# Optimization experiments

Measured on AMD Instinct MI355X. Metric: run time of the kernel, lower is better.

Reference implementation:

```python
import jax, jax.numpy as jnp
import numpy as np

K = 9            # connections per output pixel
GA = 2           # global additional samples
RA = 2           # relative additional samples
VS = 4 + GA + RA # 2^rank neighbours + sampled
REGION = 12      # int(0.25 * 48) per spatial dim
MMULT = 0.1
MIN_SIGMA = 0.05
SIGMA_SCALE = 0.05
SIGMA_BOOST = 2.0


def setup_inputs() -> dict:
    key = jax.random.key(0)
    ks = jax.random.split(key, 8)
    b, cin, h, w = 8, 128, 48, 48
    cout = 256
    hidden = cin * 4

    def lin_init(k, fan_out, fan_in):
        bound = 1.0 / np.sqrt(fan_in)
        kw, kb = jax.random.split(k)
        W = jax.random.uniform(kw, (fan_out, fan_in), minval=-bound, maxval=bound, dtype=jnp.float32)
        bb = jax.random.uniform(kb, (fan_out,), minval=-bound, maxval=bound, dtype=jnp.float32)
        return W, bb

    x = jax.random.normal(ks[0], (b, cin, h, w), dtype=jnp.float32)
    W1, b1 = lin_init(ks[1], hidden, 2)          # toparams layer 1 (adaptive=False -> 2 coord inputs)
    W2, b2 = lin_init(ks[2], 3 * K, hidden)      # toparams layer 2 -> k means (2d) + k sigmas
    Wu, bu = lin_init(ks[3], cout, K * cin)      # unify linear
    gints = jax.random.randint(ks[4], (b, h, w, K, GA, 2), 0, h, dtype=jnp.int32)      # global samples (h==w)
    roff = jax.random.randint(ks[5], (b, h, w, K, RA, 2), 0, REGION, dtype=jnp.int32)  # relative offsets
    return {"x": x, "W1": W1, "b1": b1, "W2": W2, "b2": b2, "Wu": Wu, "bu": bu,
            "gints": gints, "roff": roff}


def reference(x, W1, b1, W2, b2, Wu, bu, gints, roff):
    b, c, h, w = x.shape
    s = jnp.array([h, w], dtype=x.dtype)                       # spatial range per dim
    s_int = jnp.array([h, w], dtype=jnp.int32)

    # normalized coordinate grid in [0,1], (h, w, 2) with [.,.,0]=row, [.,.,1]=col
    rows = jnp.arange(h, dtype=x.dtype) / (h - 1)
    cols = jnp.arange(w, dtype=x.dtype) / (w - 1)
    coords = jnp.stack(jnp.meshgrid(rows, cols, indexing='ij'), axis=-1)

    # hypernetwork: per-pixel coords -> K 2d mean offsets + K sigmas
    inp = jnp.broadcast_to(coords, (b, h, w, 2))
    hid = jax.nn.relu(inp @ W1.T + b1)
    params = hid @ W2.T + b2                                   # (b,h,w,3K)
    means_raw = params[..., :2 * K].reshape(b, h, w, K, 2)
    sig_raw = params[..., 2 * K:]                              # (b,h,w,K)

    # mids: inverse of the sigmoid scaling applied to the pixel's own coordinate
    pix = coords * (s - 1)                                     # pixel coordinates
    sc = pix / (s - 1) * 0.9999 + 0.00005
    mids = jnp.log(sc / (1.0 - sc))                            # (h,w,2)

    # transform_means: sigmoid -> [0, s-1]
    means = jax.nn.sigmoid(mids[None, :, :, None, :] + MMULT * means_raw) * (s - 1)  # (b,h,w,K,2)
    # transform_sigmas: softplus(. + boost) + min, per-dim scale, then sigma_scale
    sigmas = (jax.nn.softplus(sig_raw + SIGMA_BOOST) + MIN_SIGMA)[..., None] * s * SIGMA_SCALE  # (b,h,w,K,2)

    # ---- integer index generation (non-differentiable) ----
    fl = jnp.floor(jax.lax.stop_gradient(means)).astype(jnp.int32)   # (b,h,w,K,2)
    combos = jnp.array([[0, 0], [0, 1], [1, 0], [1, 1]], dtype=jnp.int32)
    neigh = fl[..., None, :] + combos                                 # (b,h,w,K,4,2)
    rel = fl[..., None, :] + roff - REGION // 2                       # (b,h,w,K,RA,2)
    ints = jnp.concatenate([neigh, gints, rel], axis=-2) % s_int      # (b,h,w,K,VS,2)

    # duplicate masking: zero any tuple that occurred earlier along VS
    eq = jnp.all(ints[..., :, None, :] == ints[..., None, :, :], axis=-1)  # (...,VS,VS)
    lower = jnp.tril(jnp.ones((VS, VS), dtype=bool), k=-1)
    dups = jnp.any(eq & lower, axis=-1)                               # (b,h,w,K,VS)

    # unnormalized gaussian densities of integer points under (means, sigmas)
    diff = (ints.astype(x.dtype) - means[..., None, :]) / sigmas[..., None, :]
    props = jnp.exp(-0.5 * jnp.sum(diff * diff, axis=-1))             # (b,h,w,K,VS)
    props = jnp.where(dups, jnp.zeros((), x.dtype), props)
    weights = props / jnp.sum(props, axis=-1, keepdims=True)          # mvalues are all-ones

    # irregular gather of input channel vectors at sampled pixels
    lin = ints[..., 0] * w + ints[..., 1]                             # (b,h,w,K,VS)
    flat = x.transpose(0, 2, 3, 1).reshape(b, h * w, c)
    feats = flat[jnp.arange(b)[:, None], lin.reshape(b, -1)]          # (b, h*w*K*VS, c)
    feats = feats.reshape(b, h, w, K, VS, c)

    feats = jnp.einsum('bhwkvc,bhwkv->bhwkc', feats, weights)         # weighted reduce over VS
    feats = feats.reshape(b, h, w, K * c)
    out = feats @ Wu.T + bu                                           # unify linear
    return out.transpose(0, 3, 1, 2)                                  # (b, cout, h, w)
```

## Files before the change

### kernel.cpp

```cpp
#include <hip/hip_runtime.h>
#include <hip/hip_bf16.h>
#include <hip/hip_fp16.h>

#define BB 8
#define CIN 128
#define HH 48
#define WW 48
#define HW 2304
#define KK 9
#define COUT 256
#define KC 1152
#define MM 18432
#define MT 16
#define SFP 136

#define LIGHT_BARRIER() asm volatile("s_waitcnt lgkmcnt(0)\n\ts_barrier" ::: "memory")

typedef short bf16x8_t __attribute__((ext_vector_type(8)));
typedef float f32x4_t  __attribute__((ext_vector_type(4)));

static __device__ __forceinline__ float b2f(short u) {
    union { unsigned int i; float f; } c;
    c.i = ((unsigned int)(unsigned short)u) << 16;
    return c.f;
}

__global__ __launch_bounds__(256) void prep_kernel(
    const float* __restrict__ x, __hip_bfloat16* __restrict__ xT,
    const float* __restrict__ Wu, bf16x8_t* __restrict__ Bp,
    const float* __restrict__ W1, const float* __restrict__ b1,
    const float* __restrict__ W2, const float* __restrict__ b2,
    float* __restrict__ means, float* __restrict__ sigmas, int* __restrict__ fls)
{
    int bid = blockIdx.x;
    int t = threadIdx.x;

    if (bid < 576) {
        __shared__ float tile[64][65];
        int ij0 = (bid % 36) * 64;
        int c0  = ((bid / 36) % 2) * 64;
        int b   = bid / 72;
        int ijl = t & 63, cl = t >> 6;
        #pragma unroll
        for (int i = 0; i < 16; i++) {
            int cc = i*4 + cl;
            tile[cc][ijl] = x[(size_t)(b*CIN + c0 + cc) * HW + ij0 + ijl];
        }
        __syncthreads();
        int cl2 = t & 63, ijl2 = t >> 6;
        #pragma unroll
        for (int i = 0; i < 16; i++) {
            int ij = i*4 + ijl2;
            xT[(size_t)(b*HW + ij0 + ij) * CIN + c0 + cl2] = __float2bfloat16(tile[cl2][ij]);
        }
    } else if (bid < 720) {
        int idx = (bid - 576) * 256 + t;
        int lane = idx & 63;
        int rest = idx >> 6;
        int ksub = rest % 36, tile16 = rest / 36;
        const float* src = Wu + (size_t)(tile16*16 + (lane & 15)) * KC
                              + ksub*32 + (lane >> 4)*8;
        union { bf16x8_t v; __hip_bfloat16 h[8]; } o;
        #pragma unroll
        for (int j = 0; j < 8; j++) o.h[j] = __float2bfloat16(src[j]);
        Bp[idx] = o.v;
    } else {
        int wave = t >> 6, lane = t & 63;
        int p = (bid - 720) * 4 + wave;
        int iy = p / WW, ix = p % WW;
        float ryf = (float)iy / 47.0f;
        float rxf = (float)ix / 47.0f;
        double ry = (double)ryf, rx = (double)rxf;

        double h[8];
        #pragma unroll
        for (int jj = 0; jj < 8; jj++) {
            int j = lane*8 + jj;
            double v = ry * (double)W1[j*2+0] + rx * (double)W1[j*2+1] + (double)b1[j];
            h[jj] = v > 0.0 ? v : 0.0;
        }
        double par[27];
        #pragma unroll
        for (int o = 0; o < 27; o++) {
            const float4* w4 = (const float4*)(W2 + (size_t)o*512 + lane*8);
            float4 wa = w4[0], wb = w4[1];
            double s = (double)wa.x*h[0] + (double)wa.y*h[1]
                     + (double)wa.z*h[2] + (double)wa.w*h[3]
                     + (double)wb.x*h[4] + (double)wb.y*h[5]
                     + (double)wb.z*h[6] + (double)wb.w*h[7];
            par[o] = s;
        }
        #pragma unroll
        for (int o = 0; o < 27; o++) {
            #pragma unroll
            for (int d = 1; d < 64; d <<= 1)
                par[o] += __shfl_xor(par[o], d, 64);
            par[o] += (double)b2[o];
        }
        if (lane < KK) {
            int k = lane;
            double scy = ry * 0.9999 + 5e-05;
            double scx = rx * 0.9999 + 5e-05;
            double midy = log(scy / (1.0 - scy));
            double midx = log(scx / (1.0 - scx));
            double zy = midy + 0.1 * par[2*k+0];
            double zx = midx + 0.1 * par[2*k+1];
            double my = 47.0 / (1.0 + exp(-zy));
            double mx = 47.0 / (1.0 + exp(-zx));
            double sr = par[18 + k] + 2.0;
            double sp = (sr > 0.0 ? sr : 0.0) + log1p(exp(-fabs(sr)));
            double sg = (sp + 0.05) * 48.0 * 0.05;
            means[(p*KK + k)*2 + 0] = (float)my;
            means[(p*KK + k)*2 + 1] = (float)mx;
            sigmas[p*KK + k] = (float)sg;
            fls[(p*KK + k)*2 + 0] = (int)floor(my);
            fls[(p*KK + k)*2 + 1] = (int)floor(mx);
        }
    }
}

__global__ __launch_bounds__(256, 4) void fused_kernel(
    const float* __restrict__ means, const float* __restrict__ sigmas,
    const int* __restrict__ fls, const int* __restrict__ gints,
    const int* __restrict__ roff, const short* __restrict__ xT,
    const bf16x8_t* __restrict__ Bp, const float* __restrict__ bu,
    float* __restrict__ out)
{
    __shared__ unsigned int s_tap[KK*MT*8];
    __shared__ __align__(16) short s_feat[2][MT*SFP];

    int t = threadIdx.x;
    int b   = blockIdx.x & 7;
    int grp = blockIdx.x >> 3;
    int ij0 = grp * MT;
    int m0  = b * HW + ij0;

    if (t < KK*MT) {
        int p = t;
        int k = p >> 4, row = p & 15;
        int ij = ij0 + row;
        int bij = m0 + row;
        int fy = fls[(ij*KK + k)*2 + 0];
        int fx = fls[(ij*KK + k)*2 + 1];
        float my = means[(ij*KK + k)*2 + 0];
        float mx = means[(ij*KK + k)*2 + 1];
        float sg = sigmas[ij*KK + k];
        int lins[8]; float ws[8];
        #pragma unroll
        for (int v = 0; v < 8; v++) {
            int iy, ix;
            if (v < 4) {
                iy = fy + (v >> 1); ix = fx + (v & 1);
            } else if (v < 6) {
                int base = ((bij*KK + k)*2 + (v - 4)) * 2;
                iy = gints[base]; ix = gints[base + 1];
            } else {
                int base = ((bij*KK + k)*2 + (v - 6)) * 2;
                iy = fy + roff[base] - 6; ix = fx + roff[base + 1] - 6;
            }
            iy = ((iy % HH) + HH) % HH;
            ix = ((ix % WW) + WW) % WW;
            lins[v] = iy * WW + ix;
            float dy = ((float)iy - my) / sg;
            float dx = ((float)ix - mx) / sg;
            ws[v] = expf(-0.5f * (dy*dy + dx*dx));
        }
        #pragma unroll
        for (int v = 1; v < 8; v++) {
            bool dup = false;
            #pragma unroll
            for (int u = 0; u < 8; u++) if (u < v) dup = dup || (lins[u] == lins[v]);
            if (dup) ws[v] = 0.0f;
        }
        float sum = 0.0f;
        #pragma unroll
        for (int v = 0; v < 8; v++) sum += ws[v];
        float inv = 1.0f / sum;
        #pragma unroll
        for (int v = 0; v < 8; v++) {
            unsigned short hb = __half_as_ushort(__float2half(ws[v] * inv));
            s_tap[p*8+v] = ((unsigned int)lins[v] << 16) | (unsigned int)hb;
        }
    }
    LIGHT_BARRIER();

    const short* xb = xT + (size_t)b * (HW * CIN);
    int lane = t & 63, wave = t >> 6;
    int grow = t >> 4, gc0 = (t & 15) << 3;
    int arow = lane & 15, aq = lane >> 4;

    f32x4_t acc[4] = {};

    bf16x8_t tap[8];
    float    wgt[8];
    {
        const unsigned int* tp = &s_tap[(0*MT + grow)*8];
        #pragma unroll
        for (int v = 0; v < 8; v++) {
            unsigned int e = tp[v];
            wgt[v] = __half2float(__ushort_as_half((unsigned short)(e & 0xffffu)));
            tap[v] = *(const bf16x8_t*)(xb + (size_t)(e >> 16) * CIN + gc0);
        }
    }

    for (int k = 0; k < KK; k++) {
        float a0[8];
        #pragma unroll
        for (int j = 0; j < 8; j++) a0[j] = 0.0f;
        #pragma unroll
        for (int v = 0; v < 8; v++) {
            float w = wgt[v]; bf16x8_t d8 = tap[v];
            #pragma unroll
            for (int j = 0; j < 8; j++) a0[j] += w * b2f(d8[j]);
        }
        if (k < KK - 1) {
            const unsigned int* tp = &s_tap[((k+1)*MT + grow)*8];
            #pragma unroll
            for (int v = 0; v < 8; v++) {
                unsigned int e = tp[v];
                wgt[v] = __half2float(__ushort_as_half((unsigned short)(e & 0xffffu)));
                tap[v] = *(const bf16x8_t*)(xb + (size_t)(e >> 16) * CIN + gc0);
            }
        }
        {
            union { bf16x8_t v8; __hip_bfloat16 hh[8]; } o;
            #pragma unroll
            for (int j = 0; j < 8; j++) o.hh[j] = __float2bfloat16(a0[j]);
            *(bf16x8_t*)(&s_feat[k & 1][grow*SFP + gc0]) = o.v8;
        }
        LIGHT_BARRIER();
        {
            const short* fb = s_feat[k & 1];
            bf16x8_t av[4];
            #pragma unroll
            for (int s4 = 0; s4 < 4; s4++)
                av[s4] = *(const bf16x8_t*)(fb + arow*SFP + s4*32 + aq*8);
            #pragma unroll
            for (int tl = 0; tl < 4; tl++) {
                int fbase = ((wave*4 + tl)*36 + k*4)*64 + lane;
                #pragma unroll
                for (int s4 = 0; s4 < 4; s4++) {
                    bf16x8_t Bf = Bp[fbase + s4*64];
                    acc[tl] = __builtin_amdgcn_mfma_f32_16x16x32_bf16(av[s4], Bf, acc[tl], 0, 0, 0);
                }
            }
        }
    }

    #pragma unroll
    for (int tl = 0; tl < 4; tl++) {
        int n = (wave*4 + tl)*16 + arow;
        float bv = bu[n];
        f32x4_t vv;
        vv[0] = acc[tl][0] + bv;
        vv[1] = acc[tl][1] + bv;
        vv[2] = acc[tl][2] + bv;
        vv[3] = acc[tl][3] + bv;
        *(f32x4_t*)(out + ((size_t)b * COUT + n) * HW + ij0 + aq*4) = vv;
    }
}

extern "C" void kernel_launch(void* const* d_in, const int* in_sizes, int n_in,
                              void* d_out, int out_size, void* d_ws, size_t ws_size,
                              hipStream_t stream)
{
    const float* x   = (const float*)d_in[0];
    const float* W1  = (const float*)d_in[1];
    const float* b1  = (const float*)d_in[2];
    const float* W2  = (const float*)d_in[3];
    const float* b2  = (const float*)d_in[4];
    const float* Wu  = (const float*)d_in[5];
    const float* bu  = (const float*)d_in[6];
    const int* gints = (const int*)d_in[7];
    const int* roff  = (const int*)d_in[8];
    float* out = (float*)d_out;

    char* ws = (char*)d_ws;
    float* ws_means  = (float*)(ws + 0);
    float* ws_sigma  = (float*)(ws + 165888);
    int*   ws_fl     = (int*  )(ws + 248832);
    short* ws_xT     = (short*)(ws + 414720);
    bf16x8_t* ws_bp  = (bf16x8_t*)(ws + 5133312);

    prep_kernel<<<1296, 256, 0, stream>>>(x, (__hip_bfloat16*)ws_xT, Wu, ws_bp,
                                          W1, b1, W2, b2,
                                          ws_means, ws_sigma, ws_fl);
    fused_kernel<<<MM/MT, 256, 0, stream>>>(ws_means, ws_sigma, ws_fl, gints, roff,
                                            ws_xT, ws_bp, bu, out);
}
```

Before: 151.0 us.

## Double the row tile to 32 and share B fragments across two MFMA row tiles

The row tile grows from 16 to 32 pixels per block and the block from 256 to 512 threads. Each wave now computes a 2x2 grid of 16x16 MFMA tiles, so every B-fragment load from global memory feeds two row tiles instead of one, halving weight traffic per output. The tap table stride is padded from 8 to 9 words, likely to reduce LDS bank conflicts. In exchange, the grid has half as many blocks, and the tighter register budget under launch bounds of 512 threads with 4 blocks could cause spills or lower occupancy.

Result: no change. 149.7 us (-0.9%).

```diff
diff --git a/kernel.cpp b/kernel.cpp
--- a/kernel.cpp
+++ b/kernel.cpp
@@ -11,8 +11,9 @@
 #define COUT 256
 #define KC 1152
 #define MM 18432
-#define MT 16
+#define MT 32
 #define SFP 136
+#define TPS 9
 
 #define LIGHT_BARRIER() asm volatile("s_waitcnt lgkmcnt(0)\n\ts_barrier" ::: "memory")
 
@@ -119,14 +120,14 @@
     }
 }
 
-__global__ __launch_bounds__(256, 4) void fused_kernel(
+__global__ __launch_bounds__(512, 4) void fused_kernel(
     const float* __restrict__ means, const float* __restrict__ sigmas,
     const int* __restrict__ fls, const int* __restrict__ gints,
     const int* __restrict__ roff, const short* __restrict__ xT,
     const bf16x8_t* __restrict__ Bp, const float* __restrict__ bu,
     float* __restrict__ out)
 {
-    __shared__ unsigned int s_tap[KK*MT*8];
+    __shared__ unsigned int s_tap[KK*MT*TPS];
     __shared__ __align__(16) short s_feat[2][MT*SFP];
 
     int t = threadIdx.x;
@@ -137,7 +138,7 @@
 
     if (t < KK*MT) {
         int p = t;
-        int k = p >> 4, row = p & 15;
+        int k = p >> 5, row = p & 31;
         int ij = ij0 + row;
         int bij = m0 + row;
         int fy = fls[(ij*KK + k)*2 + 0];
@@ -179,7 +180,7 @@
         #pragma unroll
         for (int v = 0; v < 8; v++) {
             unsigned short hb = __half_as_ushort(__float2half(ws[v] * inv));
-            s_tap[p*8+v] = ((unsigned int)lins[v] << 16) | (unsigned int)hb;
+            s_tap[p*TPS+v] = ((unsigned int)lins[v] << 16) | (unsigned int)hb;
         }
     }
     LIGHT_BARRIER();
@@ -189,12 +190,12 @@
     int grow = t >> 4, gc0 = (t & 15) << 3;
     int arow = lane & 15, aq = lane >> 4;
 
-    f32x4_t acc[4] = {};
+    f32x4_t acc[2][2] = {};
 
     bf16x8_t tap[8];
     float    wgt[8];
     {
-        const unsigned int* tp = &s_tap[(0*MT + grow)*8];
+        const unsigned int* tp = &s_tap[(0*MT + grow)*TPS];
         #pragma unroll
         for (int v = 0; v < 8; v++) {
             unsigned int e = tp[v];
@@ -214,7 +215,7 @@
             for (int j = 0; j < 8; j++) a0[j] += w * b2f(d8[j]);
         }
         if (k < KK - 1) {
-            const unsigned int* tp = &s_tap[((k+1)*MT + grow)*8];
+            const unsigned int* tp = &s_tap[((k+1)*MT + grow)*TPS];
             #pragma unroll
             for (int v = 0; v < 8; v++) {
                 unsigned int e = tp[v];
@@ -231,32 +232,34 @@
         LIGHT_BARRIER();
         {
             const short* fb = s_feat[k & 1];
-            bf16x8_t av[4];
-            #pragma unroll
-            for (int s4 = 0; s4 < 4; s4++)
-                av[s4] = *(const bf16x8_t*)(fb + arow*SFP + s4*32 + aq*8);
-            #pragma unroll
-            for (int tl = 0; tl < 4; tl++) {
-                int fbase = ((wave*4 + tl)*36 + k*4)*64 + lane;
-                #pragma unroll
-                for (int s4 = 0; s4 < 4; s4++) {
-                    bf16x8_t Bf = Bp[fbase + s4*64];
-                    acc[tl] = __builtin_amdgcn_mfma_f32_16x16x32_bf16(av[s4], Bf, acc[tl], 0, 0, 0);
-                }
+            #pragma unroll
+            for (int s4 = 0; s4 < 4; s4++) {
+                bf16x8_t Bf0 = Bp[((wave*2 + 0)*36 + k*4 + s4)*64 + lane];
+                bf16x8_t Bf1 = Bp[((wave*2 + 1)*36 + k*4 + s4)*64 + lane];
+                bf16x8_t af0 = *(const bf16x8_t*)(fb + arow*SFP + s4*32 + aq*8);
+                bf16x8_t af1 = *(const bf16x8_t*)(fb + (16 + arow)*SFP + s4*32 + aq*8);
+                acc[0][0] = __builtin_amdgcn_mfma_f32_16x16x32_bf16(af0, Bf0, acc[0][0], 0, 0, 0);
+                acc[0][1] = __builtin_amdgcn_mfma_f32_16x16x32_bf16(af0, Bf1, acc[0][1], 0, 0, 0);
+                acc[1][0] = __builtin_amdgcn_mfma_f32_16x16x32_bf16(af1, Bf0, acc[1][0], 0, 0, 0);
+                acc[1][1] = __builtin_amdgcn_mfma_f32_16x16x32_bf16(af1, Bf1, acc[1][1], 0, 0, 0);
             }
         }
     }
 
     #pragma unroll
-    for (int tl = 0; tl < 4; tl++) {
-        int n = (wave*4 + tl)*16 + arow;
+    for (int tl = 0; tl < 2; tl++) {
+        int n = (wave*2 + tl)*16 + arow;
         float bv = bu[n];
-        f32x4_t vv;
-        vv[0] = acc[tl][0] + bv;
-        vv[1] = acc[tl][1] + bv;
-        vv[2] = acc[tl][2] + bv;
-        vv[3] = acc[tl][3] + bv;
-        *(f32x4_t*)(out + ((size_t)b * COUT + n) * HW + ij0 + aq*4) = vv;
+        float* oc = out + ((size_t)b * COUT + n) * HW + ij0;
+        #pragma unroll
+        for (int rf = 0; rf < 2; rf++) {
+            f32x4_t vv;
+            vv[0] = acc[rf][tl][0] + bv;
+            vv[1] = acc[rf][tl][1] + bv;
+            vv[2] = acc[rf][tl][2] + bv;
+            vv[3] = acc[rf][tl][3] + bv;
+            *(f32x4_t*)(oc + rf*16 + aq*4) = vv;
+        }
     }
 }
 
@@ -285,6 +288,6 @@
     prep_kernel<<<1296, 256, 0, stream>>>(x, (__hip_bfloat16*)ws_xT, Wu, ws_bp,
                                           W1, b1, W2, b2,
                                           ws_means, ws_sigma, ws_fl);
-    fused_kernel<<<MM/MT, 256, 0, stream>>>(ws_means, ws_sigma, ws_fl, gints, roff,
+    fused_kernel<<<MM/MT, 512, 0, stream>>>(ws_means, ws_sigma, ws_fl, gints, roff,
                                             ws_xT, ws_bp, bu, out);
 }
```
